# Kernel tuning notes

Hardware: AMD Instinct MI355X
Metric: run time of the kernel (lower is better)

The kernel has to match this reference:

```python
import jax, jax.numpy as jnp
import numpy as np

H_DIM = 1024
N_LAYERS = 2
N_OBJ = 64
BATCH = 512


def setup_inputs() -> dict:
    key = jax.random.key(0)
    k1, k2, k3, k4, k5, k6 = jax.random.split(key, 6)
    return {
        "obj_embed": jax.random.normal(k1, (BATCH, N_OBJ, H_DIM), dtype=jnp.float32),
        "h": jax.random.normal(k2, (1, BATCH, H_DIM), dtype=jnp.float32),
        "zeros_object": jax.random.uniform(k3, (N_OBJ, BATCH), dtype=jnp.float32),
        "t": 0,
        "W_w": jax.random.normal(k4, (H_DIM, N_LAYERS), dtype=jnp.float32) * 0.5,
        "W_ua": jax.random.normal(k5, (H_DIM, H_DIM), dtype=jnp.float32) * 0.01,
        "b_a": jnp.zeros((H_DIM,), dtype=jnp.float32),
        "W_wa": jax.random.normal(k6, (H_DIM, H_DIM), dtype=jnp.float32) * 0.01,
    }


def reference(obj_embed, h, zeros_object, t, W_w, W_ua, b_a, W_wa):
    # obj_embed: (B, n_obj, h_dim) -> (n_obj, B, h_dim)
    oe = jnp.transpose(obj_embed, (1, 0, 2))
    # image_part: (n_obj, B, h_dim)
    image_part = jnp.einsum("obh,hk->obk", oe, W_ua) + b_a
    # h: (1, B, h_dim) -> (B, 1, h_dim); d: (B, 1, h_dim)
    d = jnp.einsum("bsh,hk->bsk", jnp.transpose(h, (1, 0, 2)), W_wa)
    # broadcast (1, B, h_dim) against (n_obj, B, h_dim)
    e = jnp.tanh(jnp.transpose(d, (1, 0, 2)) + image_part)
    # scores: (n_obj, B) = sum over n_layers of e @ W_w
    scores = jnp.einsum("obh,hl->ob", e, W_w)
    alphas = jax.nn.softmax(scores, axis=0) * zeros_object * 10.0
    # weighted sum over objects -> (B, h_dim) -> (B, 1, h_dim)
    out = jnp.einsum("ob,obh->bh", alphas, oe)
    return out[:, None, :]
```

## Files before the change

kernel.cpp:

```cpp
#include <hip/hip_runtime.h>
#include <math.h>

#define H_DIM 1024
#define BATCH 512
#define NOBJ  64
#define M_TOT (NOBJ * BATCH)
#define BK 64

typedef __attribute__((ext_vector_type(8))) _Float16 half8;
typedef __attribute__((ext_vector_type(4))) float f32x4;

#define GLOAD16(gp, lp) \
    __builtin_amdgcn_global_load_lds( \
        (__attribute__((address_space(1))) const unsigned int*)(gp), \
        (__attribute__((address_space(3))) unsigned int*)(lp), 16, 0, 0)

__device__ __forceinline__ float fast_tanh(float x) {
    float e = __expf(2.0f * x);
    return 1.0f - __fdividef(2.0f, e + 1.0f);
}

__global__ __launch_bounds__(256) void kA_cvt(const float* __restrict__ obj,
                                              _Float16* __restrict__ A16) {
    const size_t i0 = ((size_t)blockIdx.x * 256 + threadIdx.x) * 16;
    const float4 v0 = *(const float4*)&obj[i0];
    const float4 v1 = *(const float4*)&obj[i0 + 4];
    const float4 v2 = *(const float4*)&obj[i0 + 8];
    const float4 v3 = *(const float4*)&obj[i0 + 12];
    half8 w0, w1;
    w0[0] = (_Float16)v0.x; w0[1] = (_Float16)v0.y;
    w0[2] = (_Float16)v0.z; w0[3] = (_Float16)v0.w;
    w0[4] = (_Float16)v1.x; w0[5] = (_Float16)v1.y;
    w0[6] = (_Float16)v1.z; w0[7] = (_Float16)v1.w;
    w1[0] = (_Float16)v2.x; w1[1] = (_Float16)v2.y;
    w1[2] = (_Float16)v2.z; w1[3] = (_Float16)v2.w;
    w1[4] = (_Float16)v3.x; w1[5] = (_Float16)v3.y;
    w1[6] = (_Float16)v3.z; w1[7] = (_Float16)v3.w;
    *(half8*)&A16[i0]     = w0;
    *(half8*)&A16[i0 + 8] = w1;
}

__global__ __launch_bounds__(256) void k0_prep(const float* __restrict__ Wua,
                                               const float* __restrict__ Ww,
                                               _Float16* __restrict__ Wh,
                                               float* __restrict__ wsum) {
    if (blockIdx.x == 0 && blockIdx.y == 0) {
        for (int i = threadIdx.x; i < H_DIM; i += 256)
            wsum[i] = Ww[i * 2] + Ww[i * 2 + 1];
    }
    __shared__ float t[64][65];
    const int k0 = blockIdx.x * 64, n0 = blockIdx.y * 64;
    #pragma unroll
    for (int it = 0; it < 4; ++it) {
        int idx = it * 256 + threadIdx.x;
        int kr = idx >> 4, nc = (idx & 15) * 4;
        *(float4*)&t[kr][nc] = *(const float4*)&Wua[(size_t)(k0 + kr) * H_DIM + n0 + nc];
    }
    __syncthreads();
    #pragma unroll
    for (int it = 0; it < 2; ++it) {
        int u = it * 256 + threadIdx.x;
        int nr = u >> 3, ku = (u & 7) * 8;
        half8 w;
        #pragma unroll
        for (int j = 0; j < 8; ++j) w[j] = (_Float16)t[ku + j][nr];
        *(half8*)&Wh[(size_t)(n0 + nr) * H_DIM + k0 + ku] = w;
    }
}

__global__ __launch_bounds__(256) void k1_dproj(const float* __restrict__ hmat,
                                                const float* __restrict__ Wwa,
                                                const float* __restrict__ ba,
                                                float* __restrict__ d2) {
    __shared__ float As[32][32];
    __shared__ float Ws[32][64];
    const int tid = threadIdx.x;
    const int m0 = blockIdx.x * 32;
    const int n0 = blockIdx.y * 64;
    const int ty = tid >> 5;
    const int tx = tid & 31;
    float acc[4][2] = {};

    for (int k0 = 0; k0 < H_DIM; k0 += 32) {
        {
            int m = tid & 31, ks = tid >> 5;
            const float4 v = *(const float4*)&hmat[(size_t)(m0 + m) * H_DIM + k0 + ks * 4];
            As[ks * 4 + 0][m] = v.x;
            As[ks * 4 + 1][m] = v.y;
            As[ks * 4 + 2][m] = v.z;
            As[ks * 4 + 3][m] = v.w;
        }
        #pragma unroll
        for (int l = 0; l < 2; ++l) {
            int u = tid + l * 256;
            int n4 = u & 15, kk = u >> 4;
            *(float4*)&Ws[kk][n4 * 4] =
                *(const float4*)&Wwa[(size_t)(k0 + kk) * H_DIM + n0 + n4 * 4];
        }
        __syncthreads();
        #pragma unroll
        for (int kk = 0; kk < 32; ++kk) {
            float av[4], bv[2];
            *(float4*)&av[0] = *(const float4*)&As[kk][ty * 4];
            bv[0] = Ws[kk][tx * 2];
            bv[1] = Ws[kk][tx * 2 + 1];
            #pragma unroll
            for (int i = 0; i < 4; ++i)
                #pragma unroll
                for (int j = 0; j < 2; ++j)
                    acc[i][j] += av[i] * bv[j];
        }
        __syncthreads();
    }
    #pragma unroll
    for (int i = 0; i < 4; ++i) {
        int r = m0 + ty * 4 + i;
        #pragma unroll
        for (int j = 0; j < 2; ++j) {
            int c = n0 + tx * 2 + j;
            d2[(size_t)r * H_DIM + c] = acc[i][j] + ba[c];
        }
    }
}

__global__ __launch_bounds__(256) void k2_scores(const _Float16* __restrict__ A16,
                                                 const _Float16* __restrict__ Wh,
                                                 const float* __restrict__ d2,
                                                 const float* __restrict__ wsum,
                                                 float* __restrict__ scores) {
    __shared__ _Float16 Asm[128 * BK];
    __shared__ _Float16 Bsm[128 * BK];

    const int hw = blockIdx.x;
    const int x  = hw & 7;
    const int j  = hw >> 3;
    const int m0 = (x * 32 + (j >> 3)) * 128;
    const int n0 = (j & 7) * 128;
    const int tid  = threadIdx.x;
    const int lane = tid & 63;
    const int wid  = tid >> 6;
    const int wr   = wid >> 1, wc = wid & 1;
    const int r    = lane & 15;
    const int g    = lane >> 4;

    const _Float16* aS[4];
    const _Float16* bS[4];
    #pragma unroll
    for (int c = 0; c < 4; ++c) {
        const int row = wid * 32 + c * 8 + (lane >> 3);
        const int u   = lane & 7;
        const int us  = (u ^ (row & 7)) * 8;
        const int m   = m0 + row;
        aS[c] = A16 + ((size_t)(m & (BATCH - 1)) * NOBJ + (m >> 9)) * H_DIM + us;
        bS[c] = Wh + (size_t)(n0 + row) * H_DIM + us;
    }

    f32x4 acc[4][4];
    #pragma unroll
    for (int i = 0; i < 4; ++i)
        #pragma unroll
        for (int jj = 0; jj < 4; ++jj)
            acc[i][jj] = (f32x4){0.f, 0.f, 0.f, 0.f};

    for (int kk0 = 0; kk0 < H_DIM; kk0 += BK) {
        #pragma unroll
        for (int c = 0; c < 4; ++c) {
            GLOAD16(aS[c] + kk0, &Asm[(wid * 32 + c * 8) * 64]);
            GLOAD16(bS[c] + kk0, &Bsm[(wid * 32 + c * 8) * 64]);
        }
        __syncthreads();

        #pragma unroll
        for (int s = 0; s < 2; ++s) {
            const int swz = ((s * 4 + g) ^ (r & 7)) * 8;
            half8 a[4], b[4];
            #pragma unroll
            for (int mi = 0; mi < 4; ++mi)
                a[mi] = *(const half8*)&Asm[(wr * 64 + mi * 16 + r) * 64 + swz];
            #pragma unroll
            for (int ni = 0; ni < 4; ++ni)
                b[ni] = *(const half8*)&Bsm[(wc * 64 + ni * 16 + r) * 64 + swz];
            #pragma unroll
            for (int mi = 0; mi < 4; ++mi)
                #pragma unroll
                for (int ni = 0; ni < 4; ++ni)
                    acc[mi][ni] = __builtin_amdgcn_mfma_f32_16x16x32_f16(
                        a[mi], b[ni], acc[mi][ni], 0, 0, 0);
        }
        __syncthreads();
    }

    float wv[4];
    int   col[4];
    #pragma unroll
    for (int ni = 0; ni < 4; ++ni) {
        col[ni] = n0 + wc * 64 + ni * 16 + r;
        wv[ni]  = wsum[col[ni]];
    }
    #pragma unroll
    for (int mi = 0; mi < 4; ++mi) {
        #pragma unroll
        for (int reg = 0; reg < 4; ++reg) {
            const int row = m0 + wr * 64 + mi * 16 + g * 4 + reg;
            const int b   = row & (BATCH - 1);
            const float* d2b = d2 + (size_t)b * H_DIM;
            float part = 0.f;
            #pragma unroll
            for (int ni = 0; ni < 4; ++ni)
                part += fast_tanh(acc[mi][ni][reg] + d2b[col[ni]]) * wv[ni];
            part += __shfl_xor(part, 1);
            part += __shfl_xor(part, 2);
            part += __shfl_xor(part, 4);
            part += __shfl_xor(part, 8);
            if (r == 0) atomicAdd(&scores[row], part);
        }
    }
}

__global__ __launch_bounds__(128) void k3_out16(const _Float16* __restrict__ A16,
                                                const float* __restrict__ scores,
                                                const float* __restrict__ zobj,
                                                float* __restrict__ out) {
    __shared__ float sc[NOBJ];
    __shared__ float al[NOBJ];
    const int b = blockIdx.x;
    const int tid = threadIdx.x;
    if (tid < NOBJ) sc[tid] = scores[(size_t)tid * BATCH + b];
    __syncthreads();
    float mx = -1e30f;
    #pragma unroll 8
    for (int o = 0; o < NOBJ; ++o) mx = fmaxf(mx, sc[o]);
    float s = 0.f;
    #pragma unroll 8
    for (int o = 0; o < NOBJ; ++o) s += expf(sc[o] - mx);
    if (tid < NOBJ)
        al[tid] = expf(sc[tid] - mx) / s * zobj[(size_t)tid * BATCH + b] * 10.0f;
    __syncthreads();

    const int h0 = tid * 8;
    float a0 = 0, a1 = 0, a2 = 0, a3 = 0, a4 = 0, a5 = 0, a6 = 0, a7 = 0;
    const _Float16* base = A16 + (size_t)b * NOBJ * H_DIM + h0;
    #pragma unroll 8
    for (int o = 0; o < NOBJ; ++o) {
        float a = al[o];
        const half8 v = *(const half8*)&base[(size_t)o * H_DIM];
        a0 += a * (float)v[0]; a1 += a * (float)v[1];
        a2 += a * (float)v[2]; a3 += a * (float)v[3];
        a4 += a * (float)v[4]; a5 += a * (float)v[5];
        a6 += a * (float)v[6]; a7 += a * (float)v[7];
    }
    float4 o0 = {a0, a1, a2, a3}, o1 = {a4, a5, a6, a7};
    *(float4*)&out[(size_t)b * H_DIM + h0]     = o0;
    *(float4*)&out[(size_t)b * H_DIM + h0 + 4] = o1;
}

__global__ __launch_bounds__(256) void k2_reg(const float* __restrict__ obj,
                                              const _Float16* __restrict__ Wh,
                                              const float* __restrict__ d2,
                                              const float* __restrict__ wsum,
                                              float* __restrict__ scores) {
    __shared__ _Float16 Asm[128 * BK];
    __shared__ _Float16 Bsm[128 * BK];
    const int hw = blockIdx.x;
    const int x  = hw & 7;
    const int j  = hw >> 3;
    const int m0 = (x * 32 + (j >> 3)) * 128;
    const int n0 = (j & 7) * 128;
    const int tid  = threadIdx.x;
    const int lane = tid & 63;
    const int wid  = tid >> 6;
    const int wr   = wid >> 1, wc = wid & 1;
    const int r    = lane & 15;
    const int g    = lane >> 4;
    const int srow = tid >> 3;
    const int su   = tid & 7;

    f32x4 acc[4][4];
    #pragma unroll
    for (int i = 0; i < 4; ++i)
        #pragma unroll
        for (int jj = 0; jj < 4; ++jj)
            acc[i][jj] = (f32x4){0.f, 0.f, 0.f, 0.f};

    for (int kk0 = 0; kk0 < H_DIM; kk0 += BK) {
        #pragma unroll
        for (int l = 0; l < 4; ++l) {
            const int row = l * 32 + srow;
            const int swz = (su ^ (row & 7)) * 8;
            {
                const int m = m0 + row;
                const size_t base = ((size_t)(m & (BATCH - 1)) * NOBJ + (m >> 9)) * H_DIM
                                    + kk0 + su * 8;
                const float4 v0 = *(const float4*)&obj[base];
                const float4 v1 = *(const float4*)&obj[base + 4];
                half8 w;
                w[0] = (_Float16)v0.x; w[1] = (_Float16)v0.y;
                w[2] = (_Float16)v0.z; w[3] = (_Float16)v0.w;
                w[4] = (_Float16)v1.x; w[5] = (_Float16)v1.y;
                w[6] = (_Float16)v1.z; w[7] = (_Float16)v1.w;
                *(half8*)&Asm[row * 64 + swz] = w;
            }
            {
                const half8 w = *(const half8*)&Wh[(size_t)(n0 + row) * H_DIM + kk0 + su * 8];
                *(half8*)&Bsm[row * 64 + swz] = w;
            }
        }
        __syncthreads();
        #pragma unroll
        for (int s = 0; s < 2; ++s) {
            const int swz = ((s * 4 + g) ^ (r & 7)) * 8;
            half8 a[4], b[4];
            #pragma unroll
            for (int mi = 0; mi < 4; ++mi)
                a[mi] = *(const half8*)&Asm[(wr * 64 + mi * 16 + r) * 64 + swz];
            #pragma unroll
            for (int ni = 0; ni < 4; ++ni)
                b[ni] = *(const half8*)&Bsm[(wc * 64 + ni * 16 + r) * 64 + swz];
            #pragma unroll
            for (int mi = 0; mi < 4; ++mi)
                #pragma unroll
                for (int ni = 0; ni < 4; ++ni)
                    acc[mi][ni] = __builtin_amdgcn_mfma_f32_16x16x32_f16(
                        a[mi], b[ni], acc[mi][ni], 0, 0, 0);
        }
        __syncthreads();
    }

    float wv[4];
    int   col[4];
    #pragma unroll
    for (int ni = 0; ni < 4; ++ni) {
        col[ni] = n0 + wc * 64 + ni * 16 + r;
        wv[ni]  = wsum[col[ni]];
    }
    #pragma unroll
    for (int mi = 0; mi < 4; ++mi) {
        #pragma unroll
        for (int reg = 0; reg < 4; ++reg) {
            const int row = m0 + wr * 64 + mi * 16 + g * 4 + reg;
            const int b   = row & (BATCH - 1);
            const float* d2b = d2 + (size_t)b * H_DIM;
            float part = 0.f;
            #pragma unroll
            for (int ni = 0; ni < 4; ++ni)
                part += fast_tanh(acc[mi][ni][reg] + d2b[col[ni]]) * wv[ni];
            part += __shfl_xor(part, 1);
            part += __shfl_xor(part, 2);
            part += __shfl_xor(part, 4);
            part += __shfl_xor(part, 8);
            if (r == 0) atomicAdd(&scores[row], part);
        }
    }
}

__global__ __launch_bounds__(128) void k3_out32(const float* __restrict__ obj,
                                                const float* __restrict__ scores,
                                                const float* __restrict__ zobj,
                                                float* __restrict__ out) {
    __shared__ float sc[NOBJ];
    __shared__ float al[NOBJ];
    const int b = blockIdx.x;
    const int tid = threadIdx.x;
    if (tid < NOBJ) sc[tid] = scores[(size_t)tid * BATCH + b];
    __syncthreads();
    float mx = -1e30f;
    #pragma unroll 8
    for (int o = 0; o < NOBJ; ++o) mx = fmaxf(mx, sc[o]);
    float s = 0.f;
    #pragma unroll 8
    for (int o = 0; o < NOBJ; ++o) s += expf(sc[o] - mx);
    if (tid < NOBJ)
        al[tid] = expf(sc[tid] - mx) / s * zobj[(size_t)tid * BATCH + b] * 10.0f;
    __syncthreads();

    const int h0 = (blockIdx.y * 128 + tid) * 4;
    float4 o4 = {0.f, 0.f, 0.f, 0.f};
    const float* base = obj + (size_t)b * NOBJ * H_DIM + h0;
    #pragma unroll 8
    for (int o = 0; o < NOBJ; ++o) {
        float a = al[o];
        float4 v = *(const float4*)&base[(size_t)o * H_DIM];
        o4.x += a * v.x;
        o4.y += a * v.y;
        o4.z += a * v.z;
        o4.w += a * v.w;
    }
    *(float4*)&out[(size_t)b * H_DIM + h0] = o4;
}

extern "C" void kernel_launch(void* const* d_in, const int* in_sizes, int n_in,
                              void* d_out, int out_size, void* d_ws, size_t ws_size,
                              hipStream_t stream) {
    const float* obj  = (const float*)d_in[0];
    const float* hmat = (const float*)d_in[1];
    const float* zobj = (const float*)d_in[2];
    const float* Ww   = (const float*)d_in[4];
    const float* Wua  = (const float*)d_in[5];
    const float* ba   = (const float*)d_in[6];
    const float* Wwa  = (const float*)d_in[7];
    float* out = (float*)d_out;

    char* ws = (char*)d_ws;
    const size_t d2_off     = 0;
    const size_t scores_off = d2_off + (size_t)BATCH * H_DIM * 4;
    const size_t wsum_off   = scores_off + (size_t)M_TOT * 4;
    const size_t Wh_off     = wsum_off + 4096;
    const size_t A16_off    = Wh_off + (size_t)H_DIM * H_DIM * 2;
    const size_t need       = A16_off + (size_t)M_TOT * H_DIM * 2;

    float*    d2     = (float*)(ws + d2_off);
    float*    scores = (float*)(ws + scores_off);
    float*    wsum   = (float*)(ws + wsum_off);
    _Float16* Wh     = (_Float16*)(ws + Wh_off);
    _Float16* A16    = (_Float16*)(ws + A16_off);

    hipMemsetAsync(scores, 0, (size_t)M_TOT * sizeof(float), stream);

    k0_prep<<<dim3(H_DIM / 64, H_DIM / 64), 256, 0, stream>>>(Wua, Ww, Wh, wsum);
    k1_dproj<<<dim3(BATCH / 32, H_DIM / 64), 256, 0, stream>>>(hmat, Wwa, ba, d2);

    if (ws_size >= need) {
        kA_cvt<<<dim3(8192), 256, 0, stream>>>(obj, A16);
        k2_scores<<<dim3((M_TOT / 128) * (H_DIM / 128)), 256, 0, stream>>>(
            A16, Wh, d2, wsum, scores);
        k3_out16<<<dim3(BATCH), 128, 0, stream>>>(A16, scores, zobj, out);
    } else {
        k2_reg<<<dim3((M_TOT / 128) * (H_DIM / 128)), 256, 0, stream>>>(
            obj, Wh, d2, wsum, scores);
        k3_out32<<<dim3(BATCH, 2), 128, 0, stream>>>(obj, scores, zobj, out);
    }
}
```

Measured before the change: 381.9 us.

## Merge prep kernels, double-buffer GEMM tiles, replace score atomics with partial buffers

Folds the fp16 conversion, weight transpose and d-projection kernels into one launch with block-index dispatch, which removes launch gaps and lets the small prep work run alongside the large conversion. The scores GEMM gains double-buffered LDS tiles, so the next K tile is loaded while MFMAs run on the current one. Atomic accumulation into scores, and the memset it needed, are replaced by per-column-tile partial sums written to a larger buffer and summed in the output kernel. The output kernel now uses 256 threads with 4 halves each. The cost is twice the LDS in the GEMM, which may lower occupancy, plus extra partial-buffer traffic.

```diff
diff --git a/kernel.cpp b/kernel.cpp
--- a/kernel.cpp
+++ b/kernel.cpp
@@ -8,6 +8,7 @@
 #define BK 64
 
 typedef __attribute__((ext_vector_type(8))) _Float16 half8;
+typedef __attribute__((ext_vector_type(4))) _Float16 half4;
 typedef __attribute__((ext_vector_type(4))) float f32x4;
 
 #define GLOAD16(gp, lp) \
@@ -20,106 +21,141 @@
     return 1.0f - __fdividef(2.0f, e + 1.0f);
 }
 
-__global__ __launch_bounds__(256) void kA_cvt(const float* __restrict__ obj,
-                                              _Float16* __restrict__ A16) {
-    const size_t i0 = ((size_t)blockIdx.x * 256 + threadIdx.x) * 16;
-    const float4 v0 = *(const float4*)&obj[i0];
-    const float4 v1 = *(const float4*)&obj[i0 + 4];
-    const float4 v2 = *(const float4*)&obj[i0 + 8];
-    const float4 v3 = *(const float4*)&obj[i0 + 12];
-    half8 w0, w1;
-    w0[0] = (_Float16)v0.x; w0[1] = (_Float16)v0.y;
-    w0[2] = (_Float16)v0.z; w0[3] = (_Float16)v0.w;
-    w0[4] = (_Float16)v1.x; w0[5] = (_Float16)v1.y;
-    w0[6] = (_Float16)v1.z; w0[7] = (_Float16)v1.w;
-    w1[0] = (_Float16)v2.x; w1[1] = (_Float16)v2.y;
-    w1[2] = (_Float16)v2.z; w1[3] = (_Float16)v2.w;
-    w1[4] = (_Float16)v3.x; w1[5] = (_Float16)v3.y;
-    w1[6] = (_Float16)v3.z; w1[7] = (_Float16)v3.w;
-    *(half8*)&A16[i0]     = w0;
-    *(half8*)&A16[i0 + 8] = w1;
-}
-
-__global__ __launch_bounds__(256) void k0_prep(const float* __restrict__ Wua,
-                                               const float* __restrict__ Ww,
-                                               _Float16* __restrict__ Wh,
-                                               float* __restrict__ wsum) {
-    if (blockIdx.x == 0 && blockIdx.y == 0) {
-        for (int i = threadIdx.x; i < H_DIM; i += 256)
-            wsum[i] = Ww[i * 2] + Ww[i * 2 + 1];
-    }
-    __shared__ float t[64][65];
-    const int k0 = blockIdx.x * 64, n0 = blockIdx.y * 64;
-    #pragma unroll
-    for (int it = 0; it < 4; ++it) {
-        int idx = it * 256 + threadIdx.x;
-        int kr = idx >> 4, nc = (idx & 15) * 4;
-        *(float4*)&t[kr][nc] = *(const float4*)&Wua[(size_t)(k0 + kr) * H_DIM + n0 + nc];
-    }
-    __syncthreads();
-    #pragma unroll
-    for (int it = 0; it < 2; ++it) {
-        int u = it * 256 + threadIdx.x;
-        int nr = u >> 3, ku = (u & 7) * 8;
-        half8 w;
-        #pragma unroll
-        for (int j = 0; j < 8; ++j) w[j] = (_Float16)t[ku + j][nr];
-        *(half8*)&Wh[(size_t)(n0 + nr) * H_DIM + k0 + ku] = w;
-    }
-}
-
-__global__ __launch_bounds__(256) void k1_dproj(const float* __restrict__ hmat,
-                                                const float* __restrict__ Wwa,
-                                                const float* __restrict__ ba,
-                                                float* __restrict__ d2) {
-    __shared__ float As[32][32];
-    __shared__ float Ws[32][64];
+__global__ __launch_bounds__(256) void k_prep(const float* __restrict__ obj,
+                                              _Float16* __restrict__ A16,
+                                              const float* __restrict__ Wua,
+                                              const float* __restrict__ Ww,
+                                              _Float16* __restrict__ Wh,
+                                              float* __restrict__ wsum,
+                                              const float* __restrict__ hmat,
+                                              const float* __restrict__ Wwa,
+                                              const float* __restrict__ ba,
+                                              float* __restrict__ d2,
+                                              int nA) {
+    __shared__ __align__(16) char smem[64 * 65 * 4];
+    const int bid = blockIdx.x;
     const int tid = threadIdx.x;
-    const int m0 = blockIdx.x * 32;
-    const int n0 = blockIdx.y * 64;
-    const int ty = tid >> 5;
-    const int tx = tid & 31;
-    float acc[4][2] = {};
-
-    for (int k0 = 0; k0 < H_DIM; k0 += 32) {
-        {
-            int m = tid & 31, ks = tid >> 5;
-            const float4 v = *(const float4*)&hmat[(size_t)(m0 + m) * H_DIM + k0 + ks * 4];
-            As[ks * 4 + 0][m] = v.x;
-            As[ks * 4 + 1][m] = v.y;
-            As[ks * 4 + 2][m] = v.z;
-            As[ks * 4 + 3][m] = v.w;
-        }
-        #pragma unroll
-        for (int l = 0; l < 2; ++l) {
-            int u = tid + l * 256;
-            int n4 = u & 15, kk = u >> 4;
-            *(float4*)&Ws[kk][n4 * 4] =
-                *(const float4*)&Wwa[(size_t)(k0 + kk) * H_DIM + n0 + n4 * 4];
+
+    if (bid < nA) {
+        const size_t i0 = ((size_t)bid * 256 + tid) * 16;
+        const float4 v0 = *(const float4*)&obj[i0];
+        const float4 v1 = *(const float4*)&obj[i0 + 4];
+        const float4 v2 = *(const float4*)&obj[i0 + 8];
+        const float4 v3 = *(const float4*)&obj[i0 + 12];
+        half8 w0, w1;
+        w0[0] = (_Float16)v0.x; w0[1] = (_Float16)v0.y;
+        w0[2] = (_Float16)v0.z; w0[3] = (_Float16)v0.w;
+        w0[4] = (_Float16)v1.x; w0[5] = (_Float16)v1.y;
+        w0[6] = (_Float16)v1.z; w0[7] = (_Float16)v1.w;
+        w1[0] = (_Float16)v2.x; w1[1] = (_Float16)v2.y;
+        w1[2] = (_Float16)v2.z; w1[3] = (_Float16)v2.w;
+        w1[4] = (_Float16)v3.x; w1[5] = (_Float16)v3.y;
+        w1[6] = (_Float16)v3.z; w1[7] = (_Float16)v3.w;
+        *(half8*)&A16[i0]     = w0;
+        *(half8*)&A16[i0 + 8] = w1;
+        return;
+    }
+
+    const int b2 = bid - nA;
+    if (b2 < 256) {
+        if (b2 == 0) {
+            for (int i = tid; i < H_DIM; i += 256)
+                wsum[i] = Ww[i * 2] + Ww[i * 2 + 1];
+        }
+        float (*t)[65] = (float(*)[65])smem;
+        const int k0 = (b2 & 15) * 64, n0 = (b2 >> 4) * 64;
+        #pragma unroll
+        for (int it = 0; it < 4; ++it) {
+            int idx = it * 256 + tid;
+            int kr = idx >> 4, nc = (idx & 15) * 4;
+            *(float4*)&t[kr][nc] = *(const float4*)&Wua[(size_t)(k0 + kr) * H_DIM + n0 + nc];
         }
         __syncthreads();
         #pragma unroll
-        for (int kk = 0; kk < 32; ++kk) {
-            float av[4], bv[2];
-            *(float4*)&av[0] = *(const float4*)&As[kk][ty * 4];
-            bv[0] = Ws[kk][tx * 2];
-            bv[1] = Ws[kk][tx * 2 + 1];
-            #pragma unroll
-            for (int i = 0; i < 4; ++i)
+        for (int it = 0; it < 2; ++it) {
+            int u = it * 256 + tid;
+            int nr = u >> 3, ku = (u & 7) * 8;
+            half8 w;
+            #pragma unroll
+            for (int j = 0; j < 8; ++j) w[j] = (_Float16)t[ku + j][nr];
+            *(half8*)&Wh[(size_t)(n0 + nr) * H_DIM + k0 + ku] = w;
+        }
+        return;
+    }
+
+    {
+        const int b1 = b2 - 256;
+        float (*As)[32] = (float(*)[32])smem;
+        float (*Ws)[64] = (float(*)[64])(smem + 4096);
+        const int m0 = (b1 & 15) * 32;
+        const int n0 = (b1 >> 4) * 64;
+        const int ty = tid >> 5;
+        const int tx = tid & 31;
+        float acc[4][2] = {};
+
+        for (int k0 = 0; k0 < H_DIM; k0 += 32) {
+            {
+                int m = tid & 31, ks = tid >> 5;
+                const float4 v = *(const float4*)&hmat[(size_t)(m0 + m) * H_DIM + k0 + ks * 4];
+                As[ks * 4 + 0][m] = v.x;
+                As[ks * 4 + 1][m] = v.y;
+                As[ks * 4 + 2][m] = v.z;
+                As[ks * 4 + 3][m] = v.w;
+            }
+            #pragma unroll
+            for (int l = 0; l < 2; ++l) {
+                int u = tid + l * 256;
+                int n4 = u & 15, kk = u >> 4;
+                *(float4*)&Ws[kk][n4 * 4] =
+                    *(const float4*)&Wwa[(size_t)(k0 + kk) * H_DIM + n0 + n4 * 4];
+            }
+            __syncthreads();
+            #pragma unroll
+            for (int kk = 0; kk < 32; ++kk) {
+                float av[4], bv[2];
+                *(float4*)&av[0] = *(const float4*)&As[kk][ty * 4];
+                bv[0] = Ws[kk][tx * 2];
+                bv[1] = Ws[kk][tx * 2 + 1];
                 #pragma unroll
-                for (int j = 0; j < 2; ++j)
-                    acc[i][j] += av[i] * bv[j];
-        }
-        __syncthreads();
-    }
-    #pragma unroll
-    for (int i = 0; i < 4; ++i) {
-        int r = m0 + ty * 4 + i;
-        #pragma unroll
-        for (int j = 0; j < 2; ++j) {
-            int c = n0 + tx * 2 + j;
-            d2[(size_t)r * H_DIM + c] = acc[i][j] + ba[c];
-        }
+                for (int i = 0; i < 4; ++i)
+                    #pragma unroll
+                    for (int j = 0; j < 2; ++j)
+                        acc[i][j] += av[i] * bv[j];
+            }
+            __syncthreads();
+        }
+        #pragma unroll
+        for (int i = 0; i < 4; ++i) {
+            int r = m0 + ty * 4 + i;
+            #pragma unroll
+            for (int j = 0; j < 2; ++j) {
+                int c = n0 + tx * 2 + j;
+                d2[(size_t)r * H_DIM + c] = acc[i][j] + ba[c];
+            }
+        }
+    }
+}
+
+__device__ __forceinline__ void k2_tile(const _Float16* __restrict__ As_,
+                                        const _Float16* __restrict__ Bs_,
+                                        int wr, int wc, int r, int g,
+                                        f32x4 acc[4][4]) {
+    #pragma unroll
+    for (int s = 0; s < 2; ++s) {
+        const int swz = ((s * 4 + g) ^ (r & 7)) * 8;
+        half8 a[4], b[4];
+        #pragma unroll
+        for (int mi = 0; mi < 4; ++mi)
+            a[mi] = *(const half8*)&As_[(wr * 64 + mi * 16 + r) * 64 + swz];
+        #pragma unroll
+        for (int ni = 0; ni < 4; ++ni)
+            b[ni] = *(const half8*)&Bs_[(wc * 64 + ni * 16 + r) * 64 + swz];
+        #pragma unroll
+        for (int mi = 0; mi < 4; ++mi)
+            #pragma unroll
+            for (int ni = 0; ni < 4; ++ni)
+                acc[mi][ni] = __builtin_amdgcn_mfma_f32_16x16x32_f16(
+                    a[mi], b[ni], acc[mi][ni], 0, 0, 0);
     }
 }
 
@@ -127,15 +163,17 @@
                                                  const _Float16* __restrict__ Wh,
                                                  const float* __restrict__ d2,
                                                  const float* __restrict__ wsum,
-                                                 float* __restrict__ scores) {
-    __shared__ _Float16 Asm[128 * BK];
-    __shared__ _Float16 Bsm[128 * BK];
+                                                 float* __restrict__ sp) {
+    __shared__ _Float16 Asm[2][128 * BK];
+    __shared__ _Float16 Bsm[2][128 * BK];
+    __shared__ float red[128];
 
     const int hw = blockIdx.x;
     const int x  = hw & 7;
     const int j  = hw >> 3;
     const int m0 = (x * 32 + (j >> 3)) * 128;
-    const int n0 = (j & 7) * 128;
+    const int jn = j & 7;
+    const int n0 = jn * 128;
     const int tid  = threadIdx.x;
     const int lane = tid & 63;
     const int wid  = tid >> 6;
@@ -162,33 +200,26 @@
         for (int jj = 0; jj < 4; ++jj)
             acc[i][jj] = (f32x4){0.f, 0.f, 0.f, 0.f};
 
-    for (int kk0 = 0; kk0 < H_DIM; kk0 += BK) {
+    #pragma unroll
+    for (int c = 0; c < 4; ++c) {
+        GLOAD16(aS[c], &Asm[0][(wid * 32 + c * 8) * 64]);
+        GLOAD16(bS[c], &Bsm[0][(wid * 32 + c * 8) * 64]);
+    }
+    __syncthreads();
+
+    int cur = 0;
+    for (int kk0 = BK; kk0 < H_DIM; kk0 += BK) {
+        const int nxt = cur ^ 1;
         #pragma unroll
         for (int c = 0; c < 4; ++c) {
-            GLOAD16(aS[c] + kk0, &Asm[(wid * 32 + c * 8) * 64]);
-            GLOAD16(bS[c] + kk0, &Bsm[(wid * 32 + c * 8) * 64]);
-        }
+            GLOAD16(aS[c] + kk0, &Asm[nxt][(wid * 32 + c * 8) * 64]);
+            GLOAD16(bS[c] + kk0, &Bsm[nxt][(wid * 32 + c * 8) * 64]);
+        }
+        k2_tile(Asm[cur], Bsm[cur], wr, wc, r, g, acc);
         __syncthreads();
-
-        #pragma unroll
-        for (int s = 0; s < 2; ++s) {
-            const int swz = ((s * 4 + g) ^ (r & 7)) * 8;
-            half8 a[4], b[4];
-            #pragma unroll
-            for (int mi = 0; mi < 4; ++mi)
-                a[mi] = *(const half8*)&Asm[(wr * 64 + mi * 16 + r) * 64 + swz];
-            #pragma unroll
-            for (int ni = 0; ni < 4; ++ni)
-                b[ni] = *(const half8*)&Bsm[(wc * 64 + ni * 16 + r) * 64 + swz];
-            #pragma unroll
-            for (int mi = 0; mi < 4; ++mi)
-                #pragma unroll
-                for (int ni = 0; ni < 4; ++ni)
-                    acc[mi][ni] = __builtin_amdgcn_mfma_f32_16x16x32_f16(
-                        a[mi], b[ni], acc[mi][ni], 0, 0, 0);
-        }
-        __syncthreads();
-    }
+        cur = nxt;
+    }
+    k2_tile(Asm[cur], Bsm[cur], wr, wc, r, g, acc);
 
     float wv[4];
     int   col[4];
@@ -197,6 +228,7 @@
         col[ni] = n0 + wc * 64 + ni * 16 + r;
         wv[ni]  = wsum[col[ni]];
     }
+    float parts[4][4];
     #pragma unroll
     for (int mi = 0; mi < 4; ++mi) {
         #pragma unroll
@@ -212,20 +244,43 @@
             part += __shfl_xor(part, 2);
             part += __shfl_xor(part, 4);
             part += __shfl_xor(part, 8);
-            if (r == 0) atomicAdd(&scores[row], part);
-        }
-    }
-}
-
-__global__ __launch_bounds__(128) void k3_out16(const _Float16* __restrict__ A16,
-                                                const float* __restrict__ scores,
+            parts[mi][reg] = part;
+        }
+    }
+    if (wc == 0 && r == 0) {
+        #pragma unroll
+        for (int mi = 0; mi < 4; ++mi)
+            #pragma unroll
+            for (int reg = 0; reg < 4; ++reg)
+                red[wr * 64 + mi * 16 + g * 4 + reg] = parts[mi][reg];
+    }
+    __syncthreads();
+    if (wc == 1 && r == 0) {
+        #pragma unroll
+        for (int mi = 0; mi < 4; ++mi)
+            #pragma unroll
+            for (int reg = 0; reg < 4; ++reg) {
+                const int lr = wr * 64 + mi * 16 + g * 4 + reg;
+                sp[(size_t)jn * M_TOT + m0 + lr] = parts[mi][reg] + red[lr];
+            }
+    }
+}
+
+__global__ __launch_bounds__(256) void k3_out16(const _Float16* __restrict__ A16,
+                                                const float* __restrict__ sp,
                                                 const float* __restrict__ zobj,
                                                 float* __restrict__ out) {
     __shared__ float sc[NOBJ];
     __shared__ float al[NOBJ];
     const int b = blockIdx.x;
     const int tid = threadIdx.x;
-    if (tid < NOBJ) sc[tid] = scores[(size_t)tid * BATCH + b];
+    if (tid < NOBJ) {
+        float s = 0.f;
+        #pragma unroll
+        for (int jn = 0; jn < 8; ++jn)
+            s += sp[(size_t)jn * M_TOT + (size_t)tid * BATCH + b];
+        sc[tid] = s;
+    }
     __syncthreads();
     float mx = -1e30f;
     #pragma unroll 8
@@ -237,21 +292,18 @@
         al[tid] = expf(sc[tid] - mx) / s * zobj[(size_t)tid * BATCH + b] * 10.0f;
     __syncthreads();
 
-    const int h0 = tid * 8;
-    float a0 = 0, a1 = 0, a2 = 0, a3 = 0, a4 = 0, a5 = 0, a6 = 0, a7 = 0;
+    const int h0 = tid * 4;
+    float a0 = 0, a1 = 0, a2 = 0, a3 = 0;
     const _Float16* base = A16 + (size_t)b * NOBJ * H_DIM + h0;
     #pragma unroll 8
     for (int o = 0; o < NOBJ; ++o) {
         float a = al[o];
-        const half8 v = *(const half8*)&base[(size_t)o * H_DIM];
+        const half4 v = *(const half4*)&base[(size_t)o * H_DIM];
         a0 += a * (float)v[0]; a1 += a * (float)v[1];
         a2 += a * (float)v[2]; a3 += a * (float)v[3];
-        a4 += a * (float)v[4]; a5 += a * (float)v[5];
-        a6 += a * (float)v[6]; a7 += a * (float)v[7];
-    }
-    float4 o0 = {a0, a1, a2, a3}, o1 = {a4, a5, a6, a7};
-    *(float4*)&out[(size_t)b * H_DIM + h0]     = o0;
-    *(float4*)&out[(size_t)b * H_DIM + h0 + 4] = o1;
+    }
+    float4 o4 = {a0, a1, a2, a3};
+    *(float4*)&out[(size_t)b * H_DIM + h0] = o4;
 }
 
 __global__ __launch_bounds__(256) void k2_reg(const float* __restrict__ obj,
@@ -306,23 +358,7 @@
             }
         }
         __syncthreads();
-        #pragma unroll
-        for (int s = 0; s < 2; ++s) {
-            const int swz = ((s * 4 + g) ^ (r & 7)) * 8;
-            half8 a[4], b[4];
-            #pragma unroll
-            for (int mi = 0; mi < 4; ++mi)
-                a[mi] = *(const half8*)&Asm[(wr * 64 + mi * 16 + r) * 64 + swz];
-            #pragma unroll
-            for (int ni = 0; ni < 4; ++ni)
-                b[ni] = *(const half8*)&Bsm[(wc * 64 + ni * 16 + r) * 64 + swz];
-            #pragma unroll
-            for (int mi = 0; mi < 4; ++mi)
-                #pragma unroll
-                for (int ni = 0; ni < 4; ++ni)
-                    acc[mi][ni] = __builtin_amdgcn_mfma_f32_16x16x32_f16(
-                        a[mi], b[ni], acc[mi][ni], 0, 0, 0);
-        }
+        k2_tile(Asm, Bsm, wr, wc, r, g, acc);
         __syncthreads();
     }
 
@@ -401,32 +437,31 @@
     float* out = (float*)d_out;
 
     char* ws = (char*)d_ws;
-    const size_t d2_off     = 0;
-    const size_t scores_off = d2_off + (size_t)BATCH * H_DIM * 4;
-    const size_t wsum_off   = scores_off + (size_t)M_TOT * 4;
-    const size_t Wh_off     = wsum_off + 4096;
-    const size_t A16_off    = Wh_off + (size_t)H_DIM * H_DIM * 2;
-    const size_t need       = A16_off + (size_t)M_TOT * H_DIM * 2;
-
-    float*    d2     = (float*)(ws + d2_off);
-    float*    scores = (float*)(ws + scores_off);
-    float*    wsum   = (float*)(ws + wsum_off);
-    _Float16* Wh     = (_Float16*)(ws + Wh_off);
-    _Float16* A16    = (_Float16*)(ws + A16_off);
-
-    hipMemsetAsync(scores, 0, (size_t)M_TOT * sizeof(float), stream);
-
-    k0_prep<<<dim3(H_DIM / 64, H_DIM / 64), 256, 0, stream>>>(Wua, Ww, Wh, wsum);
-    k1_dproj<<<dim3(BATCH / 32, H_DIM / 64), 256, 0, stream>>>(hmat, Wwa, ba, d2);
+    const size_t d2_off   = 0;
+    const size_t sp_off   = d2_off + (size_t)BATCH * H_DIM * 4;
+    const size_t wsum_off = sp_off + (size_t)8 * M_TOT * 4;
+    const size_t Wh_off   = wsum_off + 4096;
+    const size_t A16_off  = Wh_off + (size_t)H_DIM * H_DIM * 2;
+    const size_t need     = A16_off + (size_t)M_TOT * H_DIM * 2;
+
+    float*    d2   = (float*)(ws + d2_off);
+    float*    sp   = (float*)(ws + sp_off);
+    float*    wsum = (float*)(ws + wsum_off);
+    _Float16* Wh   = (_Float16*)(ws + Wh_off);
+    _Float16* A16  = (_Float16*)(ws + A16_off);
 
     if (ws_size >= need) {
-        kA_cvt<<<dim3(8192), 256, 0, stream>>>(obj, A16);
+        k_prep<<<dim3(8192 + 512), 256, 0, stream>>>(obj, A16, Wua, Ww, Wh, wsum,
+                                                     hmat, Wwa, ba, d2, 8192);
         k2_scores<<<dim3((M_TOT / 128) * (H_DIM / 128)), 256, 0, stream>>>(
-            A16, Wh, d2, wsum, scores);
-        k3_out16<<<dim3(BATCH), 128, 0, stream>>>(A16, scores, zobj, out);
+            A16, Wh, d2, wsum, sp);
+        k3_out16<<<dim3(BATCH), 256, 0, stream>>>(A16, sp, zobj, out);
     } else {
+        hipMemsetAsync(sp, 0, (size_t)M_TOT * sizeof(float), stream);
+        k_prep<<<dim3(512), 256, 0, stream>>>(obj, A16, Wua, Ww, Wh, wsum,
+                                              hmat, Wwa, ba, d2, 0);
         k2_reg<<<dim3((M_TOT / 128) * (H_DIM / 128)), 256, 0, stream>>>(
-            obj, Wh, d2, wsum, scores);
-        k3_out32<<<dim3(BATCH, 2), 128, 0, stream>>>(obj, scores, zobj, out);
-    }
-}
+            obj, Wh, d2, wsum, sp);
+        k3_out32<<<dim3(BATCH, 2), 128, 0, stream>>>(obj, sp, zobj, out);
+    }
+}
```

New measurement: 366.8 us. -3.9%, faster.
